# Optimization experiments

Measured on AMD Instinct MI355X. Metric: run time of the kernel, lower is better.

## Reference

```python
import jax, jax.numpy as jnp
import numpy as np

N_HEAD = 8
TOKEN_CODIM = 4   # mixer token codimension; attention uses per-channel tokens (codim 1)
TEMP = 1.0
EPS = 1e-5


def instance_norm(x, w=None, b=None):
    # InstanceNorm2d: normalize each (sample, channel) over spatial dims
    mu = jnp.mean(x, axis=(-2, -1), keepdims=True)
    var = jnp.var(x, axis=(-2, -1), keepdims=True)
    y = (x - mu) * jax.lax.rsqrt(var + EPS)
    if w is not None:
        y = y * w[:, None, None] + b[:, None, None]
    return y


def spectral_conv(x, wr, wi, bias, out_hw):
    # x: (B, Cin, H, W); weight (Cin, Cout, m1, m2) complex; fft_norm='forward'
    B, Cin, H, W = x.shape
    Ho, Wo = out_hw
    w = wr + 1j * wi
    m1, m2 = wr.shape[2], wr.shape[3]
    h = m1 // 2
    xf = jnp.fft.rfft2(x, norm='forward')                  # (B, Cin, H, W//2+1)
    top = jnp.einsum('bixy,ioxy->boxy', xf[:, :, :h, :m2], w[:, :, :h])
    bot = jnp.einsum('bixy,ioxy->boxy', xf[:, :, H - h:, :m2], w[:, :, h:])
    of = jnp.zeros((B, wr.shape[1], Ho, Wo // 2 + 1), dtype=xf.dtype)
    of = of.at[:, :, :h, :m2].set(top)
    of = of.at[:, :, Ho - h:, :m2].set(bot)
    return jnp.fft.irfft2(of, s=(Ho, Wo), norm='forward') + bias[:, None, None]


def fft_resample(x, Ho, Wo):
    # Fourier-truncation resampling (used for the skip branch when the conv rescales)
    B, C, H, W = x.shape
    xf = jnp.fft.rfft2(x, norm='forward')
    h, wc = Ho // 2, Wo // 2 + 1
    of = jnp.zeros((B, C, Ho, wc), dtype=xf.dtype)
    of = of.at[:, :, :h].set(xf[:, :, :h, :wc])
    of = of.at[:, :, Ho - h:].set(xf[:, :, H - h:, :wc])
    return jnp.fft.irfft2(of, s=(Ho, Wo), norm='forward')


def fno_layer(x, wr, wi, bias, sw, sb, out_hw, norm=False, act=False):
    # one FNOBlocks layer: spectral conv (+optional instance norm) + 1x1 linear skip (+act)
    skip = jnp.einsum('bihw,oi->bohw', x, sw) + sb[:, None, None]
    if out_hw != tuple(x.shape[-2:]):
        skip = fft_resample(skip, *out_hw)
    xf = spectral_conv(x, wr, wi, bias, out_hw)
    if norm:
        xf = instance_norm(xf)
    y = xf + skip
    return jax.nn.gelu(y, approximate=False) if act else y


def to_heads(z, b):
    # '(b t) (a d) h w -> b a t (d h w)'
    bt, ad, h, w = z.shape
    t = bt // b
    z = z.reshape(b, t, N_HEAD, ad // N_HEAD, h, w)
    return jnp.transpose(z, (0, 2, 1, 3, 4, 5)).reshape(b, N_HEAD, t, -1)


def setup_inputs():
    key = jax.random.key(0)
    ks = jax.random.split(key, 12)
    b, C, H, W = 2, 128, 128, 128
    f = jax.random.normal
    return dict(
        x=f(ks[0], (b, C, H, W), jnp.float32),
        norm1_w=jnp.ones((1,)), norm1_b=jnp.zeros((1,)),
        kqv_wr=f(ks[1], (3, 1, N_HEAD, 16, 8)) * 0.02,
        kqv_wi=f(ks[2], (3, 1, N_HEAD, 16, 8)) * 0.02,
        kqv_bias=f(ks[3], (3, N_HEAD)) * 0.02,
        kqv_sw=f(ks[4], (3, N_HEAD, 1)) * 0.5,
        kqv_sb=jnp.zeros((3, N_HEAD)),
        p_wr=f(ks[5], (N_HEAD, 1, 32, 16)) * 0.02,
        p_wi=f(ks[6], (N_HEAD, 1, 32, 16)) * 0.02,
        p_bias=jnp.zeros((1,)),
        p_sw=f(ks[7], (1, N_HEAD)) * (1.0 / np.sqrt(N_HEAD)),
        p_sb=jnp.zeros((1,)),
        attn_norm_w=jnp.ones((1,)), attn_norm_b=jnp.zeros((1,)),
        norm2_w=jnp.ones((TOKEN_CODIM,)), norm2_b=jnp.zeros((TOKEN_CODIM,)),
        mix_wr=f(ks[8], (2, TOKEN_CODIM, TOKEN_CODIM, 32, 16)) * 0.02,
        mix_wi=f(ks[9], (2, TOKEN_CODIM, TOKEN_CODIM, 32, 16)) * 0.02,
        mix_bias=jnp.zeros((2, TOKEN_CODIM)),
        mix_sw=f(ks[10], (2, TOKEN_CODIM, TOKEN_CODIM)) * 0.5,
        mix_sb=jnp.zeros((2, TOKEN_CODIM)),
        mon_w=jnp.ones((TOKEN_CODIM,)), mon_b=jnp.zeros((TOKEN_CODIM,)),
    )


def reference(x, norm1_w, norm1_b, kqv_wr, kqv_wi, kqv_bias, kqv_sw, kqv_sb,
              p_wr, p_wi, p_bias, p_sw, p_sb, attn_norm_w, attn_norm_b,
              norm2_w, norm2_b, mix_wr, mix_wi, mix_bias, mix_sw, mix_sb,
              mon_w, mon_b):
    b, C, H, W = x.shape
    tokens = x.reshape(b * C, 1, H, W)                     # per-channel tokens
    tok_n = instance_norm(tokens, norm1_w, norm1_b)        # norm1

    # K, Q downsampled by scale=2; V at full resolution (kqv_modes = n_modes // 2)
    k = fno_layer(tok_n, kqv_wr[0], kqv_wi[0], kqv_bias[0], kqv_sw[0], kqv_sb[0], (H // 2, W // 2))
    q = fno_layer(tok_n, kqv_wr[1], kqv_wi[1], kqv_bias[1], kqv_sw[1], kqv_sb[1], (H // 2, W // 2))
    v = fno_layer(tok_n, kqv_wr[2], kqv_wi[2], kqv_bias[2], kqv_sw[2], kqv_sb[2], (H, W))

    kh, qh, vh = to_heads(k, b), to_heads(q, b), to_heads(v, b)
    scores = jnp.einsum('bati,basi->bats', qh, kh) / (np.float32(np.sqrt(kh.shape[-1])) * TEMP)
    probs = jax.nn.softmax(scores, axis=-1)                # (b, heads, t, t)
    attn = jnp.einsum('bats,basi->bati', probs, vh)        # (b, heads, C, H*W)
    attn = attn.reshape(b, N_HEAD, C, 1, H, W).transpose(0, 2, 1, 3, 4, 5).reshape(b * C, N_HEAD, H, W)

    attn = fno_layer(attn, p_wr, p_wi, p_bias, p_sw, p_sb, (H, W))   # proj heads -> codim 1
    attn = instance_norm(attn + tokens, attn_norm_w, attn_norm_b)

    # regroup channels into mixer tokens of codimension 4
    attn = attn.reshape(b * (C // TOKEN_CODIM), TOKEN_CODIM, H, W)
    h0 = instance_norm(attn, norm2_w, norm2_b)
    h1 = fno_layer(h0, mix_wr[0], mix_wi[0], mix_bias[0], mix_sw[0], mix_sb[0], (H, W), norm=True, act=True)
    h2 = fno_layer(h1, mix_wr[1], mix_wi[1], mix_bias[1], mix_sw[1], mix_sb[1], (H, W), norm=True)
    out = instance_norm(h2, mon_w, mon_b) + attn
    return out.reshape(b, C, H, W)
```

## Files before the change

### kernel.cpp

```cpp
#include <hip/hip_runtime.h>
#include <math.h>


#define NT 2112

__device__ __forceinline__ void blockReduce2(float& a, float& b, float* red){
  const int tid = threadIdx.x, n = blockDim.x;
  red[tid] = a; red[n+tid] = b;
  __syncthreads();
  for(int off=n>>1; off>0; off>>=1){
    if(tid<off){ red[tid]+=red[tid+off]; red[n+tid]+=red[n+tid+off]; }
    __syncthreads();
  }
  a = red[0]; b = red[n];
  __syncthreads();
}

__device__ __forceinline__ float2 cmul_add(float2 acc, float2 w, float2 x){
  acc.x += w.x*x.x - w.y*x.y;
  acc.y += w.x*x.y + w.y*x.x;
  return acc;
}

__global__ void k_tables(float2* __restrict__ CS){
  int a = blockIdx.x, b = threadIdx.x;
  int p = (a*b)&127;
  float t = (float)p * (1.0f/64.0f);
  CS[a*128+b] = make_float2(cospif(t), sinpif(t));
}

__global__ __launch_bounds__(256) void k_instats(
    const float* __restrict__ xin, const float* __restrict__ n1w,
    const float* __restrict__ n1b, float* __restrict__ a1, float* __restrict__ b1)
{
  __shared__ float red[512];
  const int m = blockIdx.x, t = threadIdx.x;
  const float* xp = xin + (size_t)m*16384;
  float s1=0.f, s2=0.f;
  for(int i=t;i<4096;i+=256){
    float4 v = ((const float4*)xp)[i];
    s1 += v.x+v.y+v.z+v.w;
    s2 += v.x*v.x+v.y*v.y+v.z*v.z+v.w*v.w;
  }
  blockReduce2(s1,s2,red);
  if(t==0){
    float mu = s1*(1.0f/16384.0f);
    float var = s2*(1.0f/16384.0f)-mu*mu;
    float a = n1w[0]*rsqrtf(var+1e-5f);
    a1[m] = a; b1[m] = n1b[0] - mu*a;
  }
}

__global__ __launch_bounds__(256) void k_p1(
    const float* __restrict__ xin, float* __restrict__ R1r, float* __restrict__ R1i,
    const float2* __restrict__ CS)
{
  __shared__ float xl[32*129];
  __shared__ float2 csl[4224];
  const int bid = blockIdx.x;
  const int m = bid>>2, yt = bid&3;
  const int t = threadIdx.x;
  for(int i=t;i<4224;i+=256) csl[i] = CS[i];
  {
    const float4* xp4 = (const float4*)(xin + (size_t)m*16384 + yt*4096);
    for(int i4=t;i4<1024;i4+=256){
      float4 v = xp4[i4];
      int y = i4>>5, n = (i4&31)*4;
      xl[y*129+n]=v.x; xl[y*129+n+1]=v.y; xl[y*129+n+2]=v.z; xl[y*129+n+3]=v.w;
    }
  }
  __syncthreads();
  const int yl = t&31, cg = t>>5;
  const int nc = (cg==0)?5:4;
  float ar[5]={0,0,0,0,0}, ai[5]={0,0,0,0,0};
  for(int n=0;n<128;n++){
    float xv = xl[yl*129+n];
    #pragma unroll
    for(int k=0;k<5;k++){
      if(k<nc){
        float2 cs = csl[(cg+8*k)*128+n];
        ar[k] += xv*cs.x;
        ai[k] -= xv*cs.y;
      }
    }
  }
  __syncthreads();
  #pragma unroll
  for(int k=0;k<5;k++){
    if(k<nc){
      int c = cg+8*k;
      xl[yl*33+c] = ar[k];
      xl[1056 + yl*33+c] = ai[k];
    }
  }
  __syncthreads();
  const int gb = m*4224 + yt*1056;
  for(int idx=t; idx<2112; idx+=256){
    if(idx<1056) R1r[gb+idx] = xl[idx];
    else         R1i[gb+idx-1056] = xl[idx];
  }
}

__global__ __launch_bounds__(704) void k_p2(
    const float* __restrict__ R1r, const float* __restrict__ R1i,
    const float2* __restrict__ CS, const float* __restrict__ a1,
    const float* __restrict__ n1b,
    float2* __restrict__ Xt2, float2* __restrict__ Xp)
{
  __shared__ float2 Rl[128*34];
  const int m = blockIdx.x, t = threadIdx.x;
  for(int idx=t; idx<4224; idx+=704){
    int y = idx/33, c = idx - y*33;
    Rl[y*34+c] = make_float2(R1r[m*4224+idx], R1i[m*4224+idx]);
  }
  __syncthreads();
  const float sc = a1[m]*(1.0f/16384.0f);
  const int r = t&63;
  const int ky = (r<32)? r : r+64;
  #pragma unroll
  for(int k=0;k<3;k++){
    int c = (t>>6) + 11*k;
    float ar=0.f, ai=0.f;
    for(int y=0;y<128;y++){
      float2 Rv = Rl[y*34+c];
      float2 cs = CS[128 + ((ky*y)&127)];
      ar += Rv.x*cs.x + Rv.y*cs.y;
      ai += Rv.y*cs.x - Rv.x*cs.y;
    }
    int j = r*33 + c;
    float vr = ar*sc, vi = ai*sc;
    if(j==0){ vr = n1b[0]; vi = 0.f; }
    Xt2[m*NT+j] = make_float2(vr, vi);
    if(c<16 && (r<16 || r>=48)){
      int rp = (r<16)? r : r-32;
      Xp[m*512 + rp*16 + c] = make_float2(vr, vi);
    }
  }
}

__global__ __launch_bounds__(256) void k_build_k(
  const float2* __restrict__ Xt2,
  const float* __restrict__ kqv_wr, const float* __restrict__ kqv_wi,
  const float* __restrict__ kqv_bias, const float* __restrict__ kqv_sw,
  const float* __restrict__ kqv_sb,
  float2* __restrict__ Kc)
{
  __shared__ float2 T[2112];
  __shared__ float2 Ks[2112];
  const int bid = blockIdx.x;
  const int m = bid & 255, o = bid >> 8;
  const int tid = threadIdx.x;
  for(int j=tid;j<2112;j+=256) T[j] = Xt2[m*NT+j];
  __syncthreads();
  const float swK = kqv_sw[o];
  const float swQ = kqv_sw[8+o];
  for(int j=tid;j<2112;j+=256){
    int r = j/33, c = j - r*33;
    float2 X = T[j];
    float2 K = make_float2(swK*X.x, swK*X.y);
    if(c<8){
      int wrow = (r<8)? r : ((r>=56)? r-48 : -1);
      if(wrow>=0)
        K = cmul_add(K, make_float2(kqv_wr[(o*16+wrow)*8+c], kqv_wi[(o*16+wrow)*8+c]), X);
    }
    if(j==0) K.x += kqv_bias[o] + kqv_sb[o];
    Ks[j] = K;
  }
  __syncthreads();
  const size_t ob = ((size_t)(m*8+o))*NT;
  for(int j=tid;j<2112;j+=256){
    int r = j/33, c = j - r*33;
    float2 K = Ks[j];
    float wsc = 128.0f;
    if(c==0 || c==32){
      int pj = ((64-r)&63)*33 + c;
      float2 K2 = Ks[pj];
      K = make_float2(0.5f*(K.x+K2.x), 0.5f*(K.y-K2.y));
      wsc = 64.0f;
    }
    float ar = swQ, ai = 0.f;
    if(c<8){
      int wrow = (r<8)? r : ((r>=56)? r-48 : -1);
      if(wrow>=0){ ar += kqv_wr[((8+o)*16+wrow)*8+c]; ai += kqv_wi[((8+o)*16+wrow)*8+c]; }
    }
    float2 out = make_float2(wsc*(ar*K.x + ai*K.y), wsc*(ar*K.y - ai*K.x));
    if(j==0) out = make_float2(0.f, 0.f);
    Kc[ob+j] = out;
  }
}

__global__ __launch_bounds__(256) void k_scores(
  const float2* __restrict__ Xt2, const float2* __restrict__ Kc,
  float* __restrict__ Pp)
{
  __shared__ float Qs[64*52];
  __shared__ float Ks[64*52];
  const int bid = blockIdx.x;
  const int fq = bid&15, st = (bid>>4)&1, tt = (bid>>5)&1, h = (bid>>6)&7, b = bid>>9;
  const int t = threadIdx.x;
  const int tg = t>>4, sg = t&15;
  const int t0 = tt*64, s0 = st*64;
  const int f2base = fq*132;
  float acc[4][4];
  #pragma unroll
  for(int i=0;i<4;i++)
    #pragma unroll
    for(int j=0;j<4;j++) acc[i][j]=0.f;
  for(int sub=0; sub<6; sub++){
    __syncthreads();
    const int fo = f2base + sub*22;
    for(int idx=t; idx<1408; idx+=256){
      int rl = idx/22, f2 = idx - rl*22;
      float2 q = Xt2[(size_t)(b*128 + t0+rl)*NT + fo + f2];
      ((float2*)(Qs + rl*52))[f2] = q;
      float2 kk = Kc[((size_t)((b*128 + s0+rl)*8+h))*NT + fo + f2];
      ((float2*)(Ks + rl*52))[f2] = kk;
    }
    __syncthreads();
    #pragma unroll
    for(int f4=0; f4<11; f4++){
      float4 qv[4], kv[4];
      #pragma unroll
      for(int i=0;i<4;i++) qv[i] = *(const float4*)&Qs[(tg+16*i)*52 + f4*4];
      #pragma unroll
      for(int j=0;j<4;j++) kv[j] = *(const float4*)&Ks[(sg+16*j)*52 + f4*4];
      #pragma unroll
      for(int i=0;i<4;i++)
        #pragma unroll
        for(int j=0;j<4;j++)
          acc[i][j] += qv[i].x*kv[j].x + qv[i].y*kv[j].y
                     + qv[i].z*kv[j].z + qv[i].w*kv[j].w;
    }
  }
  #pragma unroll
  for(int i=0;i<4;i++){
    int tg2 = t0 + tg + 16*i;
    #pragma unroll
    for(int j=0;j<4;j++){
      int s = s0 + sg + 16*j;
      Pp[(size_t)fq*262144 + ((size_t)((b*8+h)*128+tg2))*128 + s] = acc[i][j];
    }
  }
}

__global__ __launch_bounds__(64) void k_softmax(const float* __restrict__ Pp,
                                                float* __restrict__ P){
  const int row = blockIdx.x, tid = threadIdx.x;
  size_t o = (size_t)row*128;
  float v0=0.f, v1=0.f;
  #pragma unroll
  for(int q=0;q<16;q++){
    v0 += Pp[(size_t)q*262144 + o + tid];
    v1 += Pp[(size_t)q*262144 + o + tid + 64];
  }
  float mx = fmaxf(v0,v1);
  for(int off=32; off; off>>=1) mx = fmaxf(mx, __shfl_xor(mx, off));
  float e0 = expf(v0-mx), e1 = expf(v1-mx);
  float s = e0+e1;
  for(int off=32; off; off>>=1) s += __shfl_xor(s, off);
  float inv = 1.0f/s;
  P[o+tid] = e0*inv; P[o+tid+64] = e1*inv;
}

__global__ __launch_bounds__(256) void k_peff(const float* __restrict__ P,
   const float* __restrict__ p_sw, const float* __restrict__ kqv_sw,
   const float* __restrict__ a1, float* __restrict__ PAT)
{
  const int i = blockIdx.x*256 + threadIdx.x;
  const int b = i>>14, rem = i&16383;
  const int tch = rem>>7, s = rem&127;
  float acc=0.f;
  for(int hh=0; hh<8; hh++){
    float a = p_sw[hh]*kqv_sw[16+hh];
    acc += a * P[(((size_t)(b*8+hh))<<14) + rem];
  }
  PAT[((size_t)(b*128+s))*128 + tch] = acc * a1[b*128+s];
}

__global__ __launch_bounds__(128) void k_pbeta(const float* __restrict__ P,
   const float* __restrict__ p_sw, const float* __restrict__ kqv_sw,
   const float* __restrict__ b1, float* __restrict__ pbeta)
{
  __shared__ float red[128];
  const int bid = blockIdx.x;
  const int b = bid>>7, tch = bid&127;
  const int s = threadIdx.x;
  float acc=0.f;
  for(int hh=0; hh<8; hh++){
    float a = p_sw[hh]*kqv_sw[16+hh];
    acc += a * P[((size_t)((b*8+hh)*128+tch))*128 + s];
  }
  acc *= b1[b*128+s];
  red[s] = acc; __syncthreads();
  for(int off=64; off>0; off>>=1){
    if(s<off) red[s]+=red[s+off];
    __syncthreads();
  }
  if(s==0) pbeta[bid] = red[0];
}

__global__ __launch_bounds__(512) void k_zcorr(
  const float* __restrict__ P, const float2* __restrict__ Xp,
  const float* __restrict__ kqv_wr, const float* __restrict__ kqv_wi,
  const float* __restrict__ kqv_bias, const float* __restrict__ kqv_sw, const float* __restrict__ kqv_sb,
  const float* __restrict__ p_wr, const float* __restrict__ p_wi,
  const float* __restrict__ p_bias, const float* __restrict__ p_sw, const float* __restrict__ p_sb,
  float2* __restrict__ Bc)
{
  __shared__ float4 Xs4[4096];
  __shared__ float Pl[1024];
  const int m = blockIdx.x;
  const int b = m>>7, cix = m&127;
  const int t = threadIdx.x;
  const int j = t;
  for(int idx=t; idx<1024; idx+=512){
    int o = idx>>7, s = idx&127;
    Pl[idx] = P[((size_t)((b*8+o)*128 + cix))*128 + s];
  }
  float2 z[8];
  #pragma unroll
  for(int o=0;o<8;o++) z[o] = make_float2(0.f,0.f);
  const float2* Xs = (const float2*)Xs4;
  for(int st=0; st<8; st++){
    __syncthreads();
    for(int q=t; q<4096; q+=512){
      int sl = q>>8, f4 = q&255;
      Xs4[q] = ((const float4*)(Xp + (size_t)(b*128 + st*16 + sl)*512))[f4];
    }
    __syncthreads();
    for(int sl=0; sl<16; sl++){
      int s = st*16 + sl;
      float2 xv = Xs[sl*512 + j];
      #pragma unroll
      for(int o=0;o<8;o++){
        float p = Pl[o*128+s];
        z[o].x += p*xv.x; z[o].y += p*xv.y;
      }
    }
  }
  __syncthreads();
  float2* Zl = (float2*)Xs4;
  #pragma unroll
  for(int o=0;o<8;o++) Zl[o*512 + j] = z[o];
  __syncthreads();
  {
    int r = j>>4, c = j&15;
    int ky = (r<16)? r : 96+r;
    float accr=0.f, acci=0.f;
    int rp = -1;
    if(c==0){ int kyp = (128-ky)&127; rp = (kyp<16)? kyp : ((kyp>=112)? kyp-96 : -1); }
    for(int o=0;o<8;o++){
      float2 zv = Zl[o*512 + j];
      float cvr=0.f, cvi=0.f;
      bool inV = (c<8) && (ky<8 || ky>=120);
      if(inV){
        int vrow = (ky<8)? ky : 8+(ky-120);
        float wr = kqv_wr[((16+o)*16+vrow)*8+c], wi = kqv_wi[((16+o)*16+vrow)*8+c];
        cvr = wr*zv.x - wi*zv.y; cvi = wr*zv.y + wi*zv.x;
      }
      float ar = cvr, ai = cvi;
      if(c==0){
        float pvr=0.f, pvi=0.f;
        int kyp = (128-ky)&127;
        bool pInV = (kyp<8 || kyp>=120);
        if(pInV && rp>=0){
          int vrow = (kyp<8)? kyp : 8+(kyp-120);
          float2 z2 = Zl[o*512 + rp*16];
          float wr = kqv_wr[((16+o)*16+vrow)*8], wi = kqv_wi[((16+o)*16+vrow)*8];
          pvr = wr*z2.x - wi*z2.y; pvi = wr*z2.y + wi*z2.x;
        }
        ar = 0.5f*(cvr + pvr);
        ai = 0.5f*(cvi - pvi);
      }
      float sv = kqv_sw[16+o];
      float Dv = kqv_bias[16+o] + kqv_sb[16+o];
      float atr = sv*zv.x + ar + ((j==0)? Dv : 0.f);
      float ati = sv*zv.y + ai;
      float psw = p_sw[o];
      accr += psw*ar;  acci += psw*ai;
      float wpr = p_wr[(o*32+r)*16+c], wpi = p_wi[(o*32+r)*16+c];
      accr += wpr*atr - wpi*ati;
      acci += wpr*ati + wpi*atr;
      if(j==0) accr += psw*Dv;
    }
    if(j==0) accr += p_bias[0] + p_sb[0];
    Bc[m*512+j] = make_float2(accr, acci);
  }
}

__global__ __launch_bounds__(256) void k_attn_gemm(
  const float* __restrict__ PAT, const float* __restrict__ xin,
  const float* __restrict__ pbeta, float* __restrict__ y0g)
{
  __shared__ float PAs[32*33];
  __shared__ float Xs[32*256];
  const int bid = blockIdx.x;
  const int b = bid>>8, ct = (bid>>6)&3, pt = bid&63;
  const int t = threadIdx.x;
  const int tc = t>>6, tp = t&63;
  float4 acc[8];
  #pragma unroll
  for(int k=0;k<8;k++) acc[k] = make_float4(0.f,0.f,0.f,0.f);
  for(int sc4=0; sc4<4; sc4++){
    __syncthreads();
    for(int idx=t; idx<1024; idx+=256){
      int sl = idx>>5, cl = idx&31;
      PAs[sl*33+cl] = PAT[((size_t)(b*128 + sc4*32+sl))*128 + ct*32+cl];
    }
    for(int q=t; q<2048; q+=256){
      int sl = q>>6, p4 = q&63;
      ((float4*)Xs)[q] =
        ((const float4*)xin)[((size_t)(b*128 + sc4*32+sl))*4096 + pt*64 + p4];
    }
    __syncthreads();
    for(int sl=0; sl<32; sl++){
      float4 xv = ((const float4*)Xs)[sl*64+tp];
      #pragma unroll
      for(int k=0;k<8;k++){
        float pa = PAs[sl*33 + tc*8+k];
        acc[k].x += pa*xv.x; acc[k].y += pa*xv.y;
        acc[k].z += pa*xv.z; acc[k].w += pa*xv.w;
      }
    }
  }
  #pragma unroll
  for(int k=0;k<8;k++){
    int c = ct*32 + tc*8 + k;
    float pb = pbeta[b*128+c];
    float4 o = acc[k];
    o.x += pb; o.y += pb; o.z += pb; o.w += pb;
    ((float4*)y0g)[((size_t)(b*128+c))*4096 + pt*64 + tp] = o;
  }
}

__global__ __launch_bounds__(512) void k_epi0(
  const float* __restrict__ y0g, const float* __restrict__ xin,
  const float2* __restrict__ Bc,
  const float2* __restrict__ CS,
  const float* __restrict__ awp, const float* __restrict__ abp,
  const float* __restrict__ n2w, const float* __restrict__ n2b,
  float* __restrict__ attn, float* __restrict__ a2, float* __restrict__ b2,
  float2* __restrict__ Hc)
{
  __shared__ float2 Bcl[512];
  __shared__ float2 V[128*17];
  __shared__ float V2p[128*132];
  __shared__ float red[1024];
  const int m = blockIdx.x, t = threadIdx.x;
  Bcl[t] = Bc[m*512+t];
  __syncthreads();
  #pragma unroll
  for(int k=0;k<4;k++){
    int idx = t + 512*k;
    int mm = idx>>4, c = idx&15;
    float vr=0.f, vi=0.f;
    for(int r=0;r<32;r++){
      int ky = (r<16)? r : 96+r;
      float2 bc = Bcl[r*16+c];
      float2 cs = CS[128 + ((ky*mm)&127)];
      vr += bc.x*cs.x - bc.y*cs.y;
      vi += bc.x*cs.y + bc.y*cs.x;
    }
    float w = (c==0)?1.0f:2.0f;
    V[mm*17+c] = make_float2(vr*w, vi*w);
  }
  __syncthreads();
  {
    const int n = t&127, mm0 = t>>7;
    float2 csr[16];
    #pragma unroll
    for(int c=0;c<16;c++) csr[c] = CS[c*128+n];
    for(int k=0;k<32;k++){
      int mm = mm0 + 4*k;
      float cv = 0.f;
      #pragma unroll
      for(int c=0;c<16;c++){
        float2 v2 = V[mm*17+c];
        cv += v2.x*csr[c].x - v2.y*csr[c].y;
      }
      V2p[mm*132+n] = cv;
    }
  }
  __syncthreads();
  const float4* x4 = (const float4*)(xin + (size_t)m*16384);
  const float4* g4 = (const float4*)(y0g + (size_t)m*16384);
  float4* V24 = (float4*)V2p;
  float s1=0.f, s2=0.f;
  for(int k=0;k<8;k++){
    int q = t + 512*k;
    int row = q>>5, c4 = q&31;
    float4 xv = x4[q], gv = g4[q], cc = V24[row*33+c4];
    float4 v;
    v.x = xv.x+gv.x+cc.x; v.y = xv.y+gv.y+cc.y;
    v.z = xv.z+gv.z+cc.z; v.w = xv.w+gv.w+cc.w;
    s1 += v.x+v.y+v.z+v.w;
    s2 += v.x*v.x+v.y*v.y+v.z*v.z+v.w*v.w;
    V24[row*33+c4] = v;
  }
  blockReduce2(s1,s2,red);
  float mu = s1*(1.0f/16384.0f);
  float var = s2*(1.0f/16384.0f)-mu*mu;
  float rs = rsqrtf(var+1e-5f);
  float aw = awp[0], ab = abp[0];
  float4* at4 = (float4*)(attn + (size_t)m*16384);
  for(int k=0;k<8;k++){
    int q = t + 512*k;
    int row = q>>5, c4 = q&31;
    float4 v = V24[row*33+c4];
    float4 ov;
    ov.x = (v.x-mu)*rs*aw + ab;
    ov.y = (v.y-mu)*rs*aw + ab;
    ov.z = (v.z-mu)*rs*aw + ab;
    ov.w = (v.w-mu)*rs*aw + ab;
    at4[q] = ov;
  }
  float va = aw*aw*var/(var+1e-5f);
  float al = n2w[m&3]*rsqrtf(va+1e-5f);
  if(t==0){ a2[m] = al; b2[m] = n2b[m&3] - ab*al; }
  __syncthreads();
  {
    const int yl = t&31, c = t>>5;
    for(int yc=0; yc<4; yc++){
      int y = yc*32+yl;
      float ar=0.f, ai=0.f;
      for(int n=0;n<128;n++){
        float zv = V2p[y*132+n];
        float2 cs = CS[c*128+n];
        ar += zv*cs.x; ai -= zv*cs.y;
      }
      V[y*17+c] = make_float2(ar, ai);
    }
  }
  __syncthreads();
  {
    const float scl = al*rs*aw*(1.0f/16384.0f);
    int idx = t;
    int r = idx>>4, c = idx&15;
    int ky = (r<16)? r : 96+r;
    float hr=0.f, hi=0.f;
    for(int y=0;y<128;y++){
      float2 Rv = V[y*17+c];
      float2 cs = CS[128 + ((ky*y)&127)];
      hr += Rv.x*cs.x + Rv.y*cs.y;
      hi += Rv.y*cs.x - Rv.x*cs.y;
    }
    float2 o = make_float2(hr*scl, hi*scl);
    if(idx==0) o = make_float2(n2b[m&3], 0.f);
    Hc[m*512+idx] = o;
  }
}

__global__ __launch_bounds__(256) void k_mixc(
  const float2* __restrict__ Hc,
  const float* __restrict__ wr0, const float* __restrict__ wi0,
  float2* __restrict__ Sn)
{
  __shared__ float2 Sl[512];
  __shared__ float red[512];
  const int mb = blockIdx.x;
  const int g = mb&63, o = mb>>6;
  const int t = threadIdx.x;
  for(int j=t;j<512;j+=256){
    int r = j>>4, c = j&15;
    float ar=0.f, ai=0.f;
    for(int i2=0;i2<4;i2++){
      float2 h = Hc[(g*4+i2)*512 + j];
      float wr = wr0[((i2*4+o)*32+r)*16+c], wi = wi0[((i2*4+o)*32+r)*16+c];
      ar += wr*h.x - wi*h.y; ai += wr*h.y + wi*h.x;
    }
    Sl[j] = make_float2(ar, ai);
  }
  __syncthreads();
  float vs=0.f, dummy=0.f;
  for(int j=t;j<512;j+=256){
    int c=j&15;
    if(c>=1) vs += 2.0f*(Sl[j].x*Sl[j].x + Sl[j].y*Sl[j].y);
  }
  if(t<32){
    int ky = (t<16)? (t+1) : (96+t);
    float ar=0.f, ai=0.f;
    if(ky<16){ ar=Sl[ky*16].x; ai=Sl[ky*16].y; }
    else if(ky>=112){ int r=ky-96; ar=Sl[r*16].x; ai=Sl[r*16].y; }
    int kyp = 128-ky;
    float br2=0.f, bi2=0.f;
    if(kyp<16){ br2=Sl[kyp*16].x; bi2=Sl[kyp*16].y; }
    else if(kyp>=112){ int r=kyp-96; br2=Sl[r*16].x; bi2=Sl[r*16].y; }
    float pr = 0.5f*(ar+br2), pi = 0.5f*(ai-bi2);
    vs += pr*pr + pi*pi;
  }
  blockReduce2(vs, dummy, red);
  float rs2 = rsqrtf(vs + 1e-5f);
  for(int j=t;j<512;j+=256){
    float2 s = Sl[j];
    if(j==0) Sn[(g*4+o)*512+j] = make_float2(0.f,0.f);
    else     Sn[(g*4+o)*512+j] = make_float2(s.x*rs2, s.y*rs2);
  }
}

__global__ __launch_bounds__(512) void k_mixinv(
  const float2* __restrict__ Sn, const float* __restrict__ inmaps,
  const float* __restrict__ a2, const float* __restrict__ b2,
  const float* __restrict__ msw, const float* __restrict__ msb,
  const float2* __restrict__ CS, const int dogelu,
  float2* __restrict__ HcOut,
  const float* __restrict__ addsrc, const float* __restrict__ mw,
  const float* __restrict__ mbv,
  float* __restrict__ outp)
{
  __shared__ float2 Sl[512];
  __shared__ float2 V[128*17];
  __shared__ float V2p[128*132];
  __shared__ float red[1024];
  const int mb = blockIdx.x;
  const int g = mb&63, o = mb>>6;
  const int mmap = g*4+o;
  const int t = threadIdx.x;
  float cw[4]; float cb = msb[o];
  #pragma unroll
  for(int i=0;i<4;i++){
    float al = a2 ? a2[g*4+i] : 1.0f;
    float be = b2 ? b2[g*4+i] : 0.0f;
    float sw = msw[o*4+i];
    cw[i] = sw*al; cb += sw*be;
  }
  Sl[t] = Sn[mmap*512+t];
  __syncthreads();
  #pragma unroll
  for(int k=0;k<4;k++){
    int idx = t + 512*k;
    int mm = idx>>4, c = idx&15;
    float vr=0.f, vi=0.f;
    for(int r=0;r<32;r++){
      int ky = (r<16)? r : 96+r;
      float2 bc = Sl[r*16+c];
      float2 cs = CS[128 + ((ky*mm)&127)];
      vr += bc.x*cs.x - bc.y*cs.y;
      vi += bc.x*cs.y + bc.y*cs.x;
    }
    float w = (c==0)?1.0f:2.0f;
    V[mm*17+c] = make_float2(vr*w, vi*w);
  }
  __syncthreads();
  {
    const int n = t&127, mm0 = t>>7;
    float2 csr[16];
    #pragma unroll
    for(int c=0;c<16;c++) csr[c] = CS[c*128+n];
    for(int k=0;k<32;k++){
      int mm = mm0 + 4*k;
      float cv = 0.f;
      #pragma unroll
      for(int c=0;c<16;c++){
        float2 v2 = V[mm*17+c];
        cv += v2.x*csr[c].x - v2.y*csr[c].y;
      }
      V2p[mm*132+n] = cv;
    }
  }
  __syncthreads();
  const float4* in4 = (const float4*)(inmaps + (size_t)(g*4)*16384);
  float4* V24 = (float4*)V2p;
  float4* o4 = (float4*)(outp + (size_t)mmap*16384);
  float s1=0.f, s2=0.f;
  for(int k=0;k<8;k++){
    int q = t + 512*k;
    int row = q>>5, c4 = q&31;
    float4 v0 = in4[q], v1 = in4[4096+q], v2 = in4[8192+q], v3 = in4[12288+q];
    float4 cc = V24[row*33+c4];
    float4 ov;
    ov.x = cb + cw[0]*v0.x + cw[1]*v1.x + cw[2]*v2.x + cw[3]*v3.x + cc.x;
    ov.y = cb + cw[0]*v0.y + cw[1]*v1.y + cw[2]*v2.y + cw[3]*v3.y + cc.y;
    ov.z = cb + cw[0]*v0.z + cw[1]*v1.z + cw[2]*v2.z + cw[3]*v3.z + cc.z;
    ov.w = cb + cw[0]*v0.w + cw[1]*v1.w + cw[2]*v2.w + cw[3]*v3.w + cc.w;
    if(dogelu){
      ov.x = 0.5f*ov.x*(1.0f+erff(ov.x*0.70710678118f));
      ov.y = 0.5f*ov.y*(1.0f+erff(ov.y*0.70710678118f));
      ov.z = 0.5f*ov.z*(1.0f+erff(ov.z*0.70710678118f));
      ov.w = 0.5f*ov.w*(1.0f+erff(ov.w*0.70710678118f));
    }
    if(addsrc){
      s1 += ov.x+ov.y+ov.z+ov.w;
      s2 += ov.x*ov.x+ov.y*ov.y+ov.z*ov.z+ov.w*ov.w;
      V24[row*33+c4] = ov;
    } else {
      o4[q] = ov;
      if(HcOut) V24[row*33+c4] = ov;
    }
  }
  if(addsrc){
    blockReduce2(s1,s2,red);
    float mu = s1*(1.0f/16384.0f);
    float var = s2*(1.0f/16384.0f)-mu*mu;
    float rs = rsqrtf(var+1e-5f);
    float w = mw[o], b = mbv[o];
    const float4* a4 = (const float4*)(addsrc + (size_t)mmap*16384);
    for(int k=0;k<8;k++){
      int q = t + 512*k;
      int row = q>>5, c4 = q&31;
      float4 v = V24[row*33+c4], av = a4[q];
      float4 ov;
      ov.x = (v.x-mu)*rs*w + b + av.x;
      ov.y = (v.y-mu)*rs*w + b + av.y;
      ov.z = (v.z-mu)*rs*w + b + av.z;
      ov.w = (v.w-mu)*rs*w + b + av.w;
      o4[q] = ov;
    }
  }
  if(HcOut){
    __syncthreads();
    {
      const int yl = t&31, c = t>>5;
      for(int yc=0; yc<4; yc++){
        int y = yc*32+yl;
        float ar=0.f, ai=0.f;
        for(int n=0;n<128;n++){
          float zv = V2p[y*132+n];
          float2 cs = CS[c*128+n];
          ar += zv*cs.x; ai -= zv*cs.y;
        }
        V[y*17+c] = make_float2(ar, ai);
      }
    }
    __syncthreads();
    {
      int idx = t;
      int r = idx>>4, c = idx&15;
      int ky = (r<16)? r : 96+r;
      float hr=0.f, hi=0.f;
      for(int y=0;y<128;y++){
        float2 Rv = V[y*17+c];
        float2 cs = CS[128 + ((ky*y)&127)];
        hr += Rv.x*cs.x + Rv.y*cs.y;
        hi += Rv.y*cs.x - Rv.x*cs.y;
      }
      HcOut[mmap*512+idx] = make_float2(hr*(1.0f/16384.0f), hi*(1.0f/16384.0f));
    }
  }
}

extern "C" void kernel_launch(void* const* d_in, const int* in_sizes, int n_in,
                              void* d_out, int out_size, void* d_ws, size_t ws_size,
                              hipStream_t stream)
{
  const float* x        = (const float*)d_in[0];
  const float* norm1_w  = (const float*)d_in[1];
  const float* norm1_b  = (const float*)d_in[2];
  const float* kqv_wr   = (const float*)d_in[3];
  const float* kqv_wi   = (const float*)d_in[4];
  const float* kqv_bias = (const float*)d_in[5];
  const float* kqv_sw   = (const float*)d_in[6];
  const float* kqv_sb   = (const float*)d_in[7];
  const float* p_wr     = (const float*)d_in[8];
  const float* p_wi     = (const float*)d_in[9];
  const float* p_bias   = (const float*)d_in[10];
  const float* p_sw     = (const float*)d_in[11];
  const float* p_sb     = (const float*)d_in[12];
  const float* attn_norm_w = (const float*)d_in[13];
  const float* attn_norm_b = (const float*)d_in[14];
  const float* norm2_w  = (const float*)d_in[15];
  const float* norm2_b  = (const float*)d_in[16];
  const float* mix_wr   = (const float*)d_in[17];
  const float* mix_wi   = (const float*)d_in[18];
  const float* mix_sw   = (const float*)d_in[20];
  const float* mix_sb   = (const float*)d_in[21];
  const float* mon_w    = (const float*)d_in[22];
  const float* mon_b    = (const float*)d_in[23];
  float* out = (float*)d_out;

  const size_t NEED = (size_t)26576128 * sizeof(float);
  if(ws_size < NEED) return;

  float* ws = (float*)d_ws;
  size_t off = 0;
  float2* CS  = (float2*)(ws + off); off += 32768;
  float* a1   = ws + off; off += 256;
  float* b1   = ws + off; off += 256;
  float* a2   = ws + off; off += 256;
  float* b2   = ws + off; off += 256;
  float* pbeta= ws + off; off += 256;
  float2* Xt2 = (float2*)(ws + off); off += 1081344;
  float* pool = ws + off; off += 17301504;
  float* P    = ws + off; off += 262144;
  float* PAT  = ws + off; off += 32768;
  float2* Xp  = (float2*)(ws + off); off += 262144;
  float* Zc_unused = ws + off; off += 2097152;
  float2* Bc  = (float2*)(ws + off); off += 262144;
  float* attn = ws + off; off += 4194304;
  float2* Hc  = (float2*)(ws + off); off += 524288;
  float2* Sn  = (float2*)(ws + off); off += 524288;
  (void)Zc_unused;

  float* Pp   = attn;

  float2* Kc = (float2*)pool;
  float* R1r = pool + 8650752;
  float* R1i = pool + 8650752 + 1081344;
  float* y0g = pool;
  float* h1  = pool + 4325376;

  k_tables<<<dim3(128), dim3(128), 0, stream>>>(CS);
  k_instats<<<dim3(256), dim3(256), 0, stream>>>(x, norm1_w, norm1_b, a1, b1);
  k_p1<<<dim3(1024), dim3(256), 0, stream>>>(x, R1r, R1i, CS);
  k_p2<<<dim3(256), dim3(704), 0, stream>>>(R1r, R1i, CS, a1, norm1_b, Xt2, Xp);
  k_build_k<<<dim3(2048), dim3(256), 0, stream>>>(Xt2, kqv_wr, kqv_wi, kqv_bias,
                                                  kqv_sw, kqv_sb, Kc);
  k_scores<<<dim3(1024), dim3(256), 0, stream>>>(Xt2, Kc, Pp);
  k_softmax<<<dim3(2048), dim3(64), 0, stream>>>(Pp, P);
  k_peff<<<dim3(128), dim3(256), 0, stream>>>(P, p_sw, kqv_sw, a1, PAT);
  k_pbeta<<<dim3(256), dim3(128), 0, stream>>>(P, p_sw, kqv_sw, b1, pbeta);
  k_zcorr<<<dim3(256), dim3(512), 0, stream>>>(P, Xp, kqv_wr, kqv_wi, kqv_bias, kqv_sw, kqv_sb,
                                               p_wr, p_wi, p_bias, p_sw, p_sb, Bc);
  k_attn_gemm<<<dim3(512), dim3(256), 0, stream>>>(PAT, x, pbeta, y0g);
  k_epi0<<<dim3(256), dim3(512), 0, stream>>>(y0g, x, Bc, CS, attn_norm_w, attn_norm_b,
                                              norm2_w, norm2_b, attn, a2, b2, Hc);
  k_mixc<<<dim3(256), dim3(256), 0, stream>>>(Hc, mix_wr, mix_wi, Sn);
  k_mixinv<<<dim3(256), dim3(512), 0, stream>>>(Sn, attn, a2, b2, mix_sw, mix_sb, CS, 1,
                                                Hc, (const float*)nullptr,
                                                (const float*)nullptr, (const float*)nullptr, h1);
  k_mixc<<<dim3(256), dim3(256), 0, stream>>>(Hc, mix_wr+8192, mix_wi+8192, Sn);
  k_mixinv<<<dim3(256), dim3(512), 0, stream>>>(Sn, h1, (const float*)nullptr, (const float*)nullptr,
                                                mix_sw+16, mix_sb+4, CS, 0,
                                                (float2*)nullptr, attn, mon_w, mon_b, out);
}
```

Baseline: 386.3 us.

## Fuse spectral mixing into inverse kernel and widen epilogue blocks to 1024 threads

Merges the k_mixc spectral channel-mix and normalization step into k_mixinv, so the mixed spectrum stays in shared memory rather than going through a global Sn buffer. This removes two kernel launches and a global round trip. It also doubles the thread count of k_epi0 and k_mixinv to 1024 and halves each thread's loop trip counts. A separate Hc2 buffer avoids the read/write alias between the two mixing layers. The risk is higher register and LDS pressure per block, plus idle threads in the 512-wide phases.

```diff
diff --git a/kernel.cpp b/kernel.cpp
--- a/kernel.cpp
+++ b/kernel.cpp
@@ -433,7 +433,7 @@
   }
 }
 
-__global__ __launch_bounds__(512) void k_epi0(
+__global__ __launch_bounds__(1024) void k_epi0(
   const float* __restrict__ y0g, const float* __restrict__ xin,
   const float2* __restrict__ Bc,
   const float2* __restrict__ CS,
@@ -445,13 +445,13 @@
   __shared__ float2 Bcl[512];
   __shared__ float2 V[128*17];
   __shared__ float V2p[128*132];
-  __shared__ float red[1024];
+  __shared__ float red[2048];
   const int m = blockIdx.x, t = threadIdx.x;
-  Bcl[t] = Bc[m*512+t];
-  __syncthreads();
-  #pragma unroll
-  for(int k=0;k<4;k++){
-    int idx = t + 512*k;
+  if(t<512) Bcl[t] = Bc[m*512+t];
+  __syncthreads();
+  #pragma unroll
+  for(int k=0;k<2;k++){
+    int idx = t + 1024*k;
     int mm = idx>>4, c = idx&15;
     float vr=0.f, vi=0.f;
     for(int r=0;r<32;r++){
@@ -470,8 +470,8 @@
     float2 csr[16];
     #pragma unroll
     for(int c=0;c<16;c++) csr[c] = CS[c*128+n];
-    for(int k=0;k<32;k++){
-      int mm = mm0 + 4*k;
+    for(int k=0;k<16;k++){
+      int mm = mm0 + 8*k;
       float cv = 0.f;
       #pragma unroll
       for(int c=0;c<16;c++){
@@ -486,8 +486,8 @@
   const float4* g4 = (const float4*)(y0g + (size_t)m*16384);
   float4* V24 = (float4*)V2p;
   float s1=0.f, s2=0.f;
-  for(int k=0;k<8;k++){
-    int q = t + 512*k;
+  for(int k=0;k<4;k++){
+    int q = t + 1024*k;
     int row = q>>5, c4 = q&31;
     float4 xv = x4[q], gv = g4[q], cc = V24[row*33+c4];
     float4 v;
@@ -503,8 +503,8 @@
   float rs = rsqrtf(var+1e-5f);
   float aw = awp[0], ab = abp[0];
   float4* at4 = (float4*)(attn + (size_t)m*16384);
-  for(int k=0;k<8;k++){
-    int q = t + 512*k;
+  for(int k=0;k<4;k++){
+    int q = t + 1024*k;
     int row = q>>5, c4 = q&31;
     float4 v = V24[row*33+c4];
     float4 ov;
@@ -519,8 +519,8 @@
   if(t==0){ a2[m] = al; b2[m] = n2b[m&3] - ab*al; }
   __syncthreads();
   {
-    const int yl = t&31, c = t>>5;
-    for(int yc=0; yc<4; yc++){
+    const int yl = t&31, c = (t>>5)&15, half = t>>9;
+    for(int yc=2*half; yc<2*half+2; yc++){
       int y = yc*32+yl;
       float ar=0.f, ai=0.f;
       for(int n=0;n<128;n++){
@@ -532,7 +532,7 @@
     }
   }
   __syncthreads();
-  {
+  if(t<512){
     const float scl = al*rs*aw*(1.0f/16384.0f);
     int idx = t;
     int r = idx>>4, c = idx&15;
@@ -550,21 +550,45 @@
   }
 }
 
-__global__ __launch_bounds__(256) void k_mixc(
-  const float2* __restrict__ Hc,
+__global__ __launch_bounds__(1024) void k_mixinv(
+  const float2* __restrict__ Hcin, const float* __restrict__ inmaps,
+  const float* __restrict__ a2, const float* __restrict__ b2,
   const float* __restrict__ wr0, const float* __restrict__ wi0,
-  float2* __restrict__ Sn)
-{
+  const float* __restrict__ msw, const float* __restrict__ msb,
+  const float2* __restrict__ CS, const int dogelu,
+  float2* __restrict__ HcOut,
+  const float* __restrict__ addsrc, const float* __restrict__ mw,
+  const float* __restrict__ mbv,
+  float* __restrict__ outp)
+{
+  __shared__ float2 Hcl[2048];
   __shared__ float2 Sl[512];
-  __shared__ float red[512];
+  __shared__ float2 V[128*17];
+  __shared__ float V2p[128*132];
+  __shared__ float red[2048];
   const int mb = blockIdx.x;
   const int g = mb&63, o = mb>>6;
+  const int mmap = g*4+o;
   const int t = threadIdx.x;
-  for(int j=t;j<512;j+=256){
-    int r = j>>4, c = j&15;
+  float cw[4]; float cb = msb[o];
+  #pragma unroll
+  for(int i=0;i<4;i++){
+    float al = a2 ? a2[g*4+i] : 1.0f;
+    float be = b2 ? b2[g*4+i] : 0.0f;
+    float sw = msw[o*4+i];
+    cw[i] = sw*al; cb += sw*be;
+  }
+  #pragma unroll
+  for(int k=0;k<2;k++){
+    int idx = t + 1024*k;
+    Hcl[idx] = Hcin[(size_t)(g*4 + (idx>>9))*512 + (idx&511)];
+  }
+  __syncthreads();
+  if(t<512){
+    int j = t, r = j>>4, c = j&15;
     float ar=0.f, ai=0.f;
     for(int i2=0;i2<4;i2++){
-      float2 h = Hc[(g*4+i2)*512 + j];
+      float2 h = Hcl[i2*512 + j];
       float wr = wr0[((i2*4+o)*32+r)*16+c], wi = wi0[((i2*4+o)*32+r)*16+c];
       ar += wr*h.x - wi*h.y; ai += wr*h.y + wi*h.x;
     }
@@ -572,9 +596,9 @@
   }
   __syncthreads();
   float vs=0.f, dummy=0.f;
-  for(int j=t;j<512;j+=256){
-    int c=j&15;
-    if(c>=1) vs += 2.0f*(Sl[j].x*Sl[j].x + Sl[j].y*Sl[j].y);
+  if(t<512){
+    int c = t&15;
+    if(c>=1) vs = 2.0f*(Sl[t].x*Sl[t].x + Sl[t].y*Sl[t].y);
   }
   if(t<32){
     int ky = (t<16)? (t+1) : (96+t);
@@ -590,44 +614,14 @@
   }
   blockReduce2(vs, dummy, red);
   float rs2 = rsqrtf(vs + 1e-5f);
-  for(int j=t;j<512;j+=256){
-    float2 s = Sl[j];
-    if(j==0) Sn[(g*4+o)*512+j] = make_float2(0.f,0.f);
-    else     Sn[(g*4+o)*512+j] = make_float2(s.x*rs2, s.y*rs2);
-  }
-}
-
-__global__ __launch_bounds__(512) void k_mixinv(
-  const float2* __restrict__ Sn, const float* __restrict__ inmaps,
-  const float* __restrict__ a2, const float* __restrict__ b2,
-  const float* __restrict__ msw, const float* __restrict__ msb,
-  const float2* __restrict__ CS, const int dogelu,
-  float2* __restrict__ HcOut,
-  const float* __restrict__ addsrc, const float* __restrict__ mw,
-  const float* __restrict__ mbv,
-  float* __restrict__ outp)
-{
-  __shared__ float2 Sl[512];
-  __shared__ float2 V[128*17];
-  __shared__ float V2p[128*132];
-  __shared__ float red[1024];
-  const int mb = blockIdx.x;
-  const int g = mb&63, o = mb>>6;
-  const int mmap = g*4+o;
-  const int t = threadIdx.x;
-  float cw[4]; float cb = msb[o];
-  #pragma unroll
-  for(int i=0;i<4;i++){
-    float al = a2 ? a2[g*4+i] : 1.0f;
-    float be = b2 ? b2[g*4+i] : 0.0f;
-    float sw = msw[o*4+i];
-    cw[i] = sw*al; cb += sw*be;
-  }
-  Sl[t] = Sn[mmap*512+t];
-  __syncthreads();
-  #pragma unroll
-  for(int k=0;k<4;k++){
-    int idx = t + 512*k;
+  if(t<512){
+    float2 s = Sl[t];
+    Sl[t] = (t==0)? make_float2(0.f,0.f) : make_float2(s.x*rs2, s.y*rs2);
+  }
+  __syncthreads();
+  #pragma unroll
+  for(int k=0;k<2;k++){
+    int idx = t + 1024*k;
     int mm = idx>>4, c = idx&15;
     float vr=0.f, vi=0.f;
     for(int r=0;r<32;r++){
@@ -646,8 +640,8 @@
     float2 csr[16];
     #pragma unroll
     for(int c=0;c<16;c++) csr[c] = CS[c*128+n];
-    for(int k=0;k<32;k++){
-      int mm = mm0 + 4*k;
+    for(int k=0;k<16;k++){
+      int mm = mm0 + 8*k;
       float cv = 0.f;
       #pragma unroll
       for(int c=0;c<16;c++){
@@ -662,8 +656,8 @@
   float4* V24 = (float4*)V2p;
   float4* o4 = (float4*)(outp + (size_t)mmap*16384);
   float s1=0.f, s2=0.f;
-  for(int k=0;k<8;k++){
-    int q = t + 512*k;
+  for(int k=0;k<4;k++){
+    int q = t + 1024*k;
     int row = q>>5, c4 = q&31;
     float4 v0 = in4[q], v1 = in4[4096+q], v2 = in4[8192+q], v3 = in4[12288+q];
     float4 cc = V24[row*33+c4];
@@ -694,8 +688,8 @@
     float rs = rsqrtf(var+1e-5f);
     float w = mw[o], b = mbv[o];
     const float4* a4 = (const float4*)(addsrc + (size_t)mmap*16384);
-    for(int k=0;k<8;k++){
-      int q = t + 512*k;
+    for(int k=0;k<4;k++){
+      int q = t + 1024*k;
       int row = q>>5, c4 = q&31;
       float4 v = V24[row*33+c4], av = a4[q];
       float4 ov;
@@ -709,8 +703,8 @@
   if(HcOut){
     __syncthreads();
     {
-      const int yl = t&31, c = t>>5;
-      for(int yc=0; yc<4; yc++){
+      const int yl = t&31, c = (t>>5)&15, half = t>>9;
+      for(int yc=2*half; yc<2*half+2; yc++){
         int y = yc*32+yl;
         float ar=0.f, ai=0.f;
         for(int n=0;n<128;n++){
@@ -722,7 +716,7 @@
       }
     }
     __syncthreads();
-    {
+    if(t<512){
       int idx = t;
       int r = idx>>4, c = idx&15;
       int ky = (r<16)? r : 96+r;
@@ -787,7 +781,7 @@
   float2* Bc  = (float2*)(ws + off); off += 262144;
   float* attn = ws + off; off += 4194304;
   float2* Hc  = (float2*)(ws + off); off += 524288;
-  float2* Sn  = (float2*)(ws + off); off += 524288;
+  float2* Hc2 = (float2*)(ws + off); off += 524288;
   (void)Zc_unused;
 
   float* Pp   = attn;
@@ -811,14 +805,13 @@
   k_zcorr<<<dim3(256), dim3(512), 0, stream>>>(P, Xp, kqv_wr, kqv_wi, kqv_bias, kqv_sw, kqv_sb,
                                                p_wr, p_wi, p_bias, p_sw, p_sb, Bc);
   k_attn_gemm<<<dim3(512), dim3(256), 0, stream>>>(PAT, x, pbeta, y0g);
-  k_epi0<<<dim3(256), dim3(512), 0, stream>>>(y0g, x, Bc, CS, attn_norm_w, attn_norm_b,
-                                              norm2_w, norm2_b, attn, a2, b2, Hc);
-  k_mixc<<<dim3(256), dim3(256), 0, stream>>>(Hc, mix_wr, mix_wi, Sn);
-  k_mixinv<<<dim3(256), dim3(512), 0, stream>>>(Sn, attn, a2, b2, mix_sw, mix_sb, CS, 1,
-                                                Hc, (const float*)nullptr,
-                                                (const float*)nullptr, (const float*)nullptr, h1);
-  k_mixc<<<dim3(256), dim3(256), 0, stream>>>(Hc, mix_wr+8192, mix_wi+8192, Sn);
-  k_mixinv<<<dim3(256), dim3(512), 0, stream>>>(Sn, h1, (const float*)nullptr, (const float*)nullptr,
-                                                mix_sw+16, mix_sb+4, CS, 0,
-                                                (float2*)nullptr, attn, mon_w, mon_b, out);
-}
+  k_epi0<<<dim3(256), dim3(1024), 0, stream>>>(y0g, x, Bc, CS, attn_norm_w, attn_norm_b,
+                                               norm2_w, norm2_b, attn, a2, b2, Hc);
+  k_mixinv<<<dim3(256), dim3(1024), 0, stream>>>(Hc, attn, a2, b2, mix_wr, mix_wi,
+                                                 mix_sw, mix_sb, CS, 1,
+                                                 Hc2, (const float*)nullptr,
+                                                 (const float*)nullptr, (const float*)nullptr, h1);
+  k_mixinv<<<dim3(256), dim3(1024), 0, stream>>>(Hc2, h1, (const float*)nullptr, (const float*)nullptr,
+                                                 mix_wr+8192, mix_wi+8192, mix_sw+16, mix_sb+4, CS, 0,
+                                                 (float2*)nullptr, attn, mon_w, mon_b, out);
+}
```

Result: faster. 376.1 us (-2.6%).
